# Performance work log

Hardware: AMD Instinct MI355X
Metric: run time of the kernel (lower is better)

Reference implementation:

```python
import jax, jax.numpy as jnp
import numpy as np

N = 50000        # nodes
E = 1600000      # edges (before self loops)
IN_DIM = 300     # input feature size
HID = 256        # hidden size
HEADS = 8
OC = HID // HEADS  # out channels per head = 32
LAYERS = 4
B = 1024         # number of target pairs
C = 3            # num classes
NEG_SLOPE = 0.2  # PyG GATConv leaky_relu slope


def setup_inputs() -> dict:
    key = jax.random.key(0)
    ks = jax.random.split(key, 12)

    def glorot(k, shape):
        lim = np.sqrt(6.0 / (shape[-2] + shape[-1]))
        return jax.random.uniform(k, shape, jnp.float32, -lim, lim)

    return {
        "x": jax.random.normal(ks[0], (N, IN_DIM), jnp.float32),
        "edge_index": jax.random.randint(ks[1], (2, E), 0, N, jnp.int64 if jax.config.jax_enable_x64 else jnp.int32),
        "target_mask": jax.random.randint(ks[2], (B, 2), 0, N, jnp.int64 if jax.config.jax_enable_x64 else jnp.int32),
        # lin1: [IN_DIM, HID] (stored pre-transposed vs torch)
        "lin1_W": glorot(ks[3], (IN_DIM, HID)),
        "lin1_b": jnp.zeros((HID,), jnp.float32),
        # stacked GATConv params
        "convs_W": glorot(ks[4], (LAYERS, HID, HEADS * OC)),
        "convs_att_dst": glorot(ks[5], (LAYERS, HEADS, OC)),  # att half applied to x_i (target)
        "convs_att_src": glorot(ks[6], (LAYERS, HEADS, OC)),  # att half applied to x_j (source)
        "convs_b": jnp.zeros((LAYERS, HID), jnp.float32),
        # lin3: [2*HID, C]
        "lin3_W": glorot(ks[7], (2 * HID, C)),
        "lin3_b": jnp.zeros((C,), jnp.float32),
    }


def gat_layer(h, src, tgt, W, att_dst, att_src, bias):
    """PyG-style GATConv (concat heads), edge list already includes self loops.
    h: [N, HID]; src/tgt: [E+N]; W: [HID, HEADS*OC]."""
    hw = (h @ W).reshape(N, HEADS, OC)
    # per-node attention scores, gathered per-edge (avoids materializing concat features)
    s_dst = jnp.einsum("nho,ho->nh", hw, att_dst)  # score for target role
    s_src = jnp.einsum("nho,ho->nh", hw, att_src)  # score for source role
    alpha = jax.nn.leaky_relu(s_dst[tgt] + s_src[src], NEG_SLOPE)  # [Etot, HEADS]
    # softmax over edges sharing the same target node (self loops => no empty segments)
    m = jax.ops.segment_max(alpha, tgt, num_segments=N)
    ex = jnp.exp(alpha - m[tgt])
    denom = jax.ops.segment_sum(ex, tgt, num_segments=N)
    a = ex / (denom[tgt] + 1e-16)
    # weighted scatter-aggregate of source features
    out = jax.ops.segment_sum(hw[src] * a[:, :, None], tgt, num_segments=N)  # [N, HEADS, OC]
    return out.reshape(N, HEADS * OC) + bias


def reference(x, edge_index, target_mask, lin1_W, lin1_b, convs_W,
              convs_att_dst, convs_att_src, convs_b, lin3_W, lin3_b):
    # add self loops once (PyG GATConv does this per layer; same edge set every layer)
    loop = jnp.arange(N, dtype=edge_index.dtype)
    src = jnp.concatenate([edge_index[0], loop])
    tgt = jnp.concatenate([edge_index[1], loop])

    h = x @ lin1_W + lin1_b
    for l in range(LAYERS):
        h = jax.nn.elu(gat_layer(h, src, tgt, convs_W[l],
                                 convs_att_dst[l], convs_att_src[l], convs_b[l]))
    # gather the two target nodes per sample and flatten -> [B, 2*HID]
    feats = h[target_mask].reshape(B, 2 * HID)
    logits = feats @ lin3_W + lin3_b
    return logits
```

## Files before the change

### kernel.cpp

```cpp
#include <hip/hip_runtime.h>
#include <math.h>

#define N_NODES 50000
#define N_PAD   50048
#define E_EDGES 1600000
#define ETOT    (E_EDGES + N_NODES)
#define EPAD    (E_EDGES + 8 * N_NODES)
#define IN_DIM  300
#define KP1     320
#define HID     256
#define HEADS   8
#define OC      32
#define LAYERS  4
#define BSAMP   1024
#define NEG_SLOPE 0.2f
#define DEG_CAP 128

#define NB     8
#define NPB    6250
#define BCAP   262144
#define NBLK_P 512
#define NBLK_S 196
#define NBLK_B 2048
#define NAGG   2048

typedef unsigned long long ull;
typedef _Float16 half8 __attribute__((ext_vector_type(8)));
typedef _Float16 half4v __attribute__((ext_vector_type(4)));
typedef float f32x4 __attribute__((ext_vector_type(4)));

#define GLDS16(g, l) __builtin_amdgcn_global_load_lds( \
    (const __attribute__((address_space(1))) void*)(g), \
    (__attribute__((address_space(3))) void*)(l), 16, 0, 0)


__global__ __launch_bounds__(256) void part_count_kernel(const int* __restrict__ tgt,
                                                         int* __restrict__ gcount) {
    __shared__ int cnt[NB];
    if (threadIdx.x < NB) cnt[threadIdx.x] = 0;
    __syncthreads();
    const int chunk = (ETOT + NBLK_P - 1) / NBLK_P;
    int beg = blockIdx.x * chunk;
    int end = min(beg + chunk, ETOT);
    for (int e = beg + threadIdx.x; e < end; e += 256) {
        int t_ = (e < E_EDGES) ? tgt[e] : (e - E_EDGES);
        atomicAdd(&cnt[t_ / NPB], 1);
    }
    __syncthreads();
    if (threadIdx.x < NB) gcount[blockIdx.x * NB + threadIdx.x] = cnt[threadIdx.x];
}

__global__ __launch_bounds__(512) void part_scan_kernel(const int* __restrict__ gcount,
                                                        int* __restrict__ goff,
                                                        int* __restrict__ bcnt) {
    __shared__ int arr[NBLK_P][NB];
    int k = threadIdx.x;
    int4 a = ((const int4*)gcount)[k * 2];
    int4 b = ((const int4*)gcount)[k * 2 + 1];
    int own[NB] = {a.x, a.y, a.z, a.w, b.x, b.y, b.z, b.w};
    #pragma unroll
    for (int j = 0; j < NB; j++) arr[k][j] = own[j];
    __syncthreads();
    for (int off = 1; off < NBLK_P; off <<= 1) {
        int tmp[NB];
        #pragma unroll
        for (int j = 0; j < NB; j++) tmp[j] = (k >= off) ? arr[k - off][j] : 0;
        __syncthreads();
        #pragma unroll
        for (int j = 0; j < NB; j++) arr[k][j] += tmp[j];
        __syncthreads();
    }
    int ex[NB];
    #pragma unroll
    for (int j = 0; j < NB; j++) ex[j] = arr[k][j] - own[j];
    ((int4*)goff)[k * 2]     = make_int4(ex[0], ex[1], ex[2], ex[3]);
    ((int4*)goff)[k * 2 + 1] = make_int4(ex[4], ex[5], ex[6], ex[7]);
    if (k == NBLK_P - 1) {
        #pragma unroll
        for (int j = 0; j < NB; j++) bcnt[j] = arr[k][j];
    }
}

__global__ __launch_bounds__(256) void part_scatter_kernel(const int* __restrict__ src,
                                                           const int* __restrict__ tgt,
                                                           const int* __restrict__ goff,
                                                           ull* __restrict__ bpart) {
    __shared__ int cur[NB];
    if (threadIdx.x < NB) cur[threadIdx.x] = goff[blockIdx.x * NB + threadIdx.x];
    __syncthreads();
    const int chunk = (ETOT + NBLK_P - 1) / NBLK_P;
    int beg = blockIdx.x * chunk;
    int end = min(beg + chunk, ETOT);
    for (int e = beg + threadIdx.x; e < end; e += 256) {
        int s_, t_;
        if (e < E_EDGES) { s_ = src[e]; t_ = tgt[e]; }
        else             { s_ = t_ = e - E_EDGES; }
        int b = t_ / NPB;
        int pos = atomicAdd(&cur[b], 1);
        bpart[(size_t)b * BCAP + pos] = ((ull)(unsigned)t_ << 32) | (unsigned)s_;
    }
}

__global__ __launch_bounds__(256) void count_edges_kernel(const ull* __restrict__ bpart,
                                                          const int* __restrict__ bcnt,
                                                          int* counts) {
    int b = blockIdx.x & (NB - 1);
    int ib = blockIdx.x >> 3;
    int nblk = gridDim.x >> 3;
    int nb = bcnt[b];
    const ull* bp = bpart + (size_t)b * BCAP;
    for (int i = ib * 256 + threadIdx.x; i < nb; i += nblk * 256)
        atomicAdd(&counts[(int)(bp[i] >> 32)], 1);
}

__global__ __launch_bounds__(256) void scan1_kernel(const int* __restrict__ counts,
                                                    int* __restrict__ row_ptr,
                                                    int* __restrict__ bsum) {
    __shared__ int sums[256];
    int t = threadIdx.x;
    int i = blockIdx.x * 256 + t;
    int c = (i < N_NODES) ? ((counts[i] + 7) & ~7) : 0;
    sums[t] = c;
    __syncthreads();
    for (int off = 1; off < 256; off <<= 1) {
        int a = sums[t];
        int u = (t >= off) ? sums[t - off] : 0;
        __syncthreads();
        sums[t] = a + u;
        __syncthreads();
    }
    if (i < N_NODES) row_ptr[i] = sums[t] - c;
    if (t == 255) bsum[blockIdx.x] = sums[255];
}

__global__ __launch_bounds__(256) void scan2_kernel(const int* __restrict__ bsum,
                                                    int* __restrict__ boff,
                                                    int* __restrict__ row_ptr) {
    __shared__ int sums[256];
    int t = threadIdx.x;
    int b = (t < NBLK_S) ? bsum[t] : 0;
    sums[t] = b;
    __syncthreads();
    for (int off = 1; off < 256; off <<= 1) {
        int a = sums[t];
        int u = (t >= off) ? sums[t - off] : 0;
        __syncthreads();
        sums[t] = a + u;
        __syncthreads();
    }
    if (t < NBLK_S) boff[t] = sums[t] - b;
    if (t == 255) row_ptr[N_NODES] = sums[255];
}

__global__ __launch_bounds__(256) void scan3_kernel(int* __restrict__ row_ptr,
                                                    const int* __restrict__ boff,
                                                    int* __restrict__ cursor) {
    int i = blockIdx.x * 256 + threadIdx.x;
    if (i >= N_NODES) return;
    int v = row_ptr[i] + boff[blockIdx.x];
    row_ptr[i] = v;
    cursor[i]  = v;
}

__global__ __launch_bounds__(256) void fill_edges_kernel(const ull* __restrict__ bpart,
                                                         const int* __restrict__ bcnt,
                                                         int* cursor, int* __restrict__ col) {
    int b = blockIdx.x & (NB - 1);
    int ib = blockIdx.x >> 3;
    int nblk = gridDim.x >> 3;
    int nb = bcnt[b];
    const ull* bp = bpart + (size_t)b * BCAP;
    for (int i = ib * 256 + threadIdx.x; i < nb; i += nblk * 256) {
        ull pk = bp[i];
        int t_ = (int)(pk >> 32);
        int s_ = (int)pk;
        int pos = atomicAdd(&cursor[t_], 1);
        col[pos] = s_;
    }
}

__global__ __launch_bounds__(256) void pad_edges_kernel(const int* __restrict__ cursor,
                                                        const int* __restrict__ row_ptr,
                                                        int* __restrict__ col) {
    int i = blockIdx.x * 256 + threadIdx.x;
    if (i >= N_NODES) return;
    int e = cursor[i];
    int pe = row_ptr[i + 1];
    for (; e < pe; e++) col[e] = i;
}


__global__ __launch_bounds__(256) void cast_x_kernel(const float* __restrict__ x, _Float16* __restrict__ xh) {
    int i = blockIdx.x * 256 + threadIdx.x;
    if (i >= N_NODES * (KP1 / 8)) return;
    int r = i / (KP1 / 8), c8 = i % (KP1 / 8);
    half8 o;
    const float4* xr = (const float4*)(x + (size_t)r * IN_DIM);
    if (c8 < 37) {
        float4 u = xr[c8 * 2], v = xr[c8 * 2 + 1];
        o[0] = (_Float16)u.x; o[1] = (_Float16)u.y; o[2] = (_Float16)u.z; o[3] = (_Float16)u.w;
        o[4] = (_Float16)v.x; o[5] = (_Float16)v.y; o[6] = (_Float16)v.z; o[7] = (_Float16)v.w;
    } else if (c8 == 37) {
        float4 u = xr[74];
        o[0] = (_Float16)u.x; o[1] = (_Float16)u.y; o[2] = (_Float16)u.z; o[3] = (_Float16)u.w;
        o[4] = o[5] = o[6] = o[7] = (_Float16)0.f;
    } else {
        #pragma unroll
        for (int j = 0; j < 8; j++) o[j] = (_Float16)0.f;
    }
    ((half8*)xh)[i] = o;
}

__global__ __launch_bounds__(256) void cast_w1_kernel(const float* __restrict__ W, _Float16* __restrict__ Wt) {
    int i = blockIdx.x * 256 + threadIdx.x;
    if (i >= HID * KP1) return;
    int n = i / KP1, k = i % KP1;
    float v = (k < IN_DIM) ? W[(size_t)k * HID + n] : 0.f;
    Wt[i] = (_Float16)v;
}

__global__ __launch_bounds__(256) void cast_wc_kernel(const float* __restrict__ W, _Float16* __restrict__ Wt) {
    int i = blockIdx.x * 256 + threadIdx.x;
    if (i >= LAYERS * HID * HID) return;
    int l = i / (HID * HID);
    int r = i % (HID * HID);
    int n = r / HID, k = r % HID;
    Wt[i] = (_Float16)W[(size_t)l * HID * HID + (size_t)k * HID + n];
}

__global__ __launch_bounds__(256) void gemm_mfma_kernel(const _Float16* __restrict__ A,
                                                        const _Float16* __restrict__ Wt,
                                                        const float* __restrict__ bias,
                                                        _Float16* __restrict__ C,
                                                        int M, int Kp, int addbias) {
    __shared__ _Float16 As[128][32];
    __shared__ _Float16 Bs[128][32];
    const int tid = threadIdx.x;
    const int m0 = blockIdx.x * 128;
    const int n0 = blockIdx.y * 128;
    const int w = tid >> 6, lane = tid & 63;
    const int wm = (w & 1) * 64, wn = (w >> 1) * 64;
    const int quad = lane >> 4, m16 = lane & 15;

    f32x4 acc[4][4];
    #pragma unroll
    for (int i = 0; i < 4; i++)
        #pragma unroll
        for (int j = 0; j < 4; j++)
            acc[i][j] = (f32x4){0.f, 0.f, 0.f, 0.f};

    char* lA = (char*)&As[0][0] + w * 1024;
    char* lB = (char*)&Bs[0][0] + w * 1024;

    for (int k0 = 0; k0 < Kp; k0 += 32) {
        #pragma unroll
        for (int i = 0; i < 2; i++) {
            int seg = tid + i * 256;
            int row = seg >> 2, off = seg & 3;
            GLDS16(&A[(size_t)(m0 + row) * Kp + k0 + off * 8], lA + i * 4096);
            GLDS16(&Wt[(size_t)(n0 + row) * Kp + k0 + off * 8], lB + i * 4096);
        }
        __syncthreads();

        half8 af[4], bf[4];
        #pragma unroll
        for (int i = 0; i < 4; i++) {
            af[i] = *(const half8*)&As[wm + i * 16 + m16][quad * 8];
            bf[i] = *(const half8*)&Bs[wn + i * 16 + m16][quad * 8];
        }
        #pragma unroll
        for (int mi = 0; mi < 4; mi++)
            #pragma unroll
            for (int ni = 0; ni < 4; ni++)
                acc[mi][ni] = __builtin_amdgcn_mfma_f32_16x16x32_f16(af[mi], bf[ni], acc[mi][ni], 0, 0, 0);
        __syncthreads();
    }

    #pragma unroll
    for (int mi = 0; mi < 4; mi++) {
        #pragma unroll
        for (int r = 0; r < 4; r++) {
            int row = m0 + wm + mi * 16 + quad * 4 + r;
            if (row < M) {
                #pragma unroll
                for (int ni = 0; ni < 4; ni++) {
                    int colg = n0 + wn + ni * 16 + m16;
                    float v = acc[mi][ni][r];
                    if (addbias) v += bias[colg];
                    C[(size_t)row * HID + colg] = (_Float16)v;
                }
            }
        }
    }
}

__global__ __launch_bounds__(256) void score_kernel(const _Float16* __restrict__ hw,
                                                    const float* __restrict__ att_dst,
                                                    const float* __restrict__ att_src,
                                                    float* __restrict__ s_dst,
                                                    float* __restrict__ s_src) {
    int wv = threadIdx.x >> 6, lane = threadIdx.x & 63;
    int nd = lane >> 3, hd = lane & 7;
    float4 ad[8], as4[8];
    const float4* A4d = (const float4*)att_dst;
    const float4* A4s = (const float4*)att_src;
    #pragma unroll
    for (int j = 0; j < 8; j++) { ad[j] = A4d[hd * 8 + j]; as4[j] = A4s[hd * 8 + j]; }
    const half8* hw8 = (const half8*)hw;
    int nwaves = gridDim.x * 4;
    for (int g = blockIdx.x * 4 + wv; g < N_NODES / 8; g += nwaves) {
        int node = g * 8 + nd;
        float sd = 0.f, ss = 0.f;
        #pragma unroll
        for (int k = 0; k < 4; k++) {
            half8 v = hw8[(size_t)node * 32 + hd * 4 + k];
            #pragma unroll
            for (int i = 0; i < 8; i++) {
                float f = (float)v[i];
                int q = k * 8 + i;
                sd += f * ((const float*)&ad[q >> 2])[q & 3];
                ss += f * ((const float*)&as4[q >> 2])[q & 3];
            }
        }
        s_dst[(size_t)g * 64 + lane] = sd;
        s_src[(size_t)g * 64 + lane] = ss;
    }
}

__global__ __launch_bounds__(256) void agg_kernel(const int* __restrict__ row_ptr,
                                                  const int* __restrict__ deg_arr,
                                                  const int* __restrict__ col,
                                                  const float* __restrict__ s_dst,
                                                  const float* __restrict__ s_src,
                                                  const _Float16* __restrict__ hw,
                                                  const float* __restrict__ bias,
                                                  _Float16* __restrict__ h_out) {
    const int wv   = threadIdx.x >> 6;
    const int lane = threadIdx.x & 63;
    const int bkt  = blockIdx.x & (NB - 1);
    const int ib   = blockIdx.x >> 3;
    const int p  = lane >> 5;
    const int c  = lane & 31;
    const int hh = c >> 2;
    const half8* hw8 = (const half8*)hw;

    f32x4 b0 = ((const f32x4*)bias)[c * 2];
    f32x4 b1 = ((const f32x4*)bias)[c * 2 + 1];

    for (int t0 = ib * 4 + wv; t0 < NPB; t0 += (NAGG / NB) * 4) {
        int t = bkt * NPB + t0;
        int start = row_ptr[t];
        int pdeg  = row_ptr[t + 1] - start;
        int deg   = deg_arr[t];

        if (pdeg <= DEG_CAP) {
            float sdC = s_dst[(size_t)t * HEADS + hh];
            int ngrp = pdeg >> 3;
            const int* cb = col + start;
            float dsum = 0.f;
            float acc[8] = {0.f, 0.f, 0.f, 0.f, 0.f, 0.f, 0.f, 0.f};

            int s0 = cb[p], s1 = cb[2 + p], s2 = cb[4 + p], s3 = cb[6 + p];

            for (int g = 0; g < ngrp; g++) {
                int base = g * 8;
                int n0 = s0, n1 = s1, n2 = s2, n3 = s3;
                if (g + 1 < ngrp) {
                    const int* nb_ = cb + base + 8;
                    n0 = nb_[p]; n1 = nb_[2 + p]; n2 = nb_[4 + p]; n3 = nb_[6 + p];
                }
                float ss0 = s_src[(size_t)s0 * HEADS + hh];
                float ss1 = s_src[(size_t)s1 * HEADS + hh];
                float ss2 = s_src[(size_t)s2 * HEADS + hh];
                float ss3 = s_src[(size_t)s3 * HEADS + hh];
                half8 v0 = hw8[(size_t)s0 * 32 + c];
                half8 v1 = hw8[(size_t)s1 * 32 + c];
                half8 v2 = hw8[(size_t)s2 * 32 + c];
                half8 v3 = hw8[(size_t)s3 * 32 + c];

                float a0 = sdC + ss0; a0 = (a0 > 0.f) ? a0 : NEG_SLOPE * a0;
                float a1 = sdC + ss1; a1 = (a1 > 0.f) ? a1 : NEG_SLOPE * a1;
                float a2 = sdC + ss2; a2 = (a2 > 0.f) ? a2 : NEG_SLOPE * a2;
                float a3 = sdC + ss3; a3 = (a3 > 0.f) ? a3 : NEG_SLOPE * a3;
                float e0 = (base + 0 + p < deg) ? __expf(a0) : 0.f;
                float e1 = (base + 2 + p < deg) ? __expf(a1) : 0.f;
                float e2 = (base + 4 + p < deg) ? __expf(a2) : 0.f;
                float e3 = (base + 6 + p < deg) ? __expf(a3) : 0.f;
                dsum += (e0 + e1) + (e2 + e3);

                #pragma unroll
                for (int i = 0; i < 8; i++)
                    acc[i] += e0 * (float)v0[i] + e1 * (float)v1[i]
                            + e2 * (float)v2[i] + e3 * (float)v3[i];

                s0 = n0; s1 = n1; s2 = n2; s3 = n3;
            }

            dsum += __shfl_xor(dsum, 32);
            float inv = 1.f / (dsum + 1e-16f);
            #pragma unroll
            for (int i = 0; i < 8; i++) acc[i] += __shfl_xor(acc[i], 32);

            if (p == 0) {
                half8 ov;
                #pragma unroll
                for (int i = 0; i < 8; i++) {
                    float bb = (i < 4) ? ((const float*)&b0)[i] : ((const float*)&b1)[i - 4];
                    float o = acc[i] * inv + bb;
                    o = (o > 0.f) ? o : (__expf(o) - 1.f);
                    ov[i] = (_Float16)o;
                }
                ((half8*)h_out)[(size_t)t * 32 + c] = ov;
            }
        } else {
            int eh  = lane & 7;
            int ech = lane >> 3;
            float sd = s_dst[(size_t)t * HEADS + eh];
            int end = start + deg;
            float mx = -1e30f;
            for (int base = start; base < end; base += 8) {
                int e = base + ech;
                if (e < end) {
                    int sn = col[e];
                    float a = sd + s_src[(size_t)sn * HEADS + eh];
                    a = (a > 0.f) ? a : NEG_SLOPE * a;
                    mx = fmaxf(mx, a);
                }
            }
            mx = fmaxf(mx, __shfl_xor(mx, 8));
            mx = fmaxf(mx, __shfl_xor(mx, 16));
            mx = fmaxf(mx, __shfl_xor(mx, 32));

            float4 acc = {0.f, 0.f, 0.f, 0.f};
            float dsum = 0.f;
            const half4v* hw4 = (const half4v*)hw;
            int chead = lane >> 3;
            for (int base = start; base < end; base += 8) {
                int e = base + ech;
                float exv = 0.f;
                int sn = 0;
                if (e < end) {
                    sn = col[e];
                    float a = sd + s_src[(size_t)sn * HEADS + eh];
                    a = (a > 0.f) ? a : NEG_SLOPE * a;
                    exv = __expf(a - mx);
                    dsum += exv;
                }
                int cnt = min(8, end - base);
                for (int j = 0; j < cnt; j++) {
                    float exj = __shfl(exv, j * 8 + chead);
                    int  snj  = __shfl(sn,  j * 8);
                    half4v v = hw4[(size_t)snj * 64 + lane];
                    acc.x += exj * (float)v[0];
                    acc.y += exj * (float)v[1];
                    acc.z += exj * (float)v[2];
                    acc.w += exj * (float)v[3];
                }
            }
            dsum += __shfl_xor(dsum, 8);
            dsum += __shfl_xor(dsum, 16);
            dsum += __shfl_xor(dsum, 32);
            float den = __shfl(dsum, chead) + 1e-16f;
            float inv = 1.f / den;
            int cb = lane * 4;
            float o[4] = {acc.x * inv + bias[cb + 0], acc.y * inv + bias[cb + 1],
                          acc.z * inv + bias[cb + 2], acc.w * inv + bias[cb + 3]};
            #pragma unroll
            for (int i = 0; i < 4; i++) o[i] = (o[i] > 0.f) ? o[i] : (__expf(o[i]) - 1.f);
            half4v ov;
            ov[0] = (_Float16)o[0]; ov[1] = (_Float16)o[1];
            ov[2] = (_Float16)o[2]; ov[3] = (_Float16)o[3];
            ((half4v*)h_out)[(size_t)t * 64 + lane] = ov;
        }
    }
}

__global__ __launch_bounds__(256) void head_kernel(const _Float16* __restrict__ h,
                                                   const int* __restrict__ target_mask,
                                                   const float* __restrict__ W,
                                                   const float* __restrict__ b,
                                                   float* __restrict__ out) {
    int s = blockIdx.x;
    int t = threadIdx.x;
    int n0 = target_mask[s * 2 + 0];
    int n1 = target_mask[s * 2 + 1];
    float f0 = (float)h[(size_t)n0 * HID + t];
    float f1 = (float)h[(size_t)n1 * HID + t];
    float a0 = f0 * W[t * 3 + 0] + f1 * W[(t + 256) * 3 + 0];
    float a1 = f0 * W[t * 3 + 1] + f1 * W[(t + 256) * 3 + 1];
    float a2 = f0 * W[t * 3 + 2] + f1 * W[(t + 256) * 3 + 2];
    #pragma unroll
    for (int off = 32; off >= 1; off >>= 1) {
        a0 += __shfl_xor(a0, off);
        a1 += __shfl_xor(a1, off);
        a2 += __shfl_xor(a2, off);
    }
    __shared__ float red[4][3];
    int wv = t >> 6, ln = t & 63;
    if (ln == 0) { red[wv][0] = a0; red[wv][1] = a1; red[wv][2] = a2; }
    __syncthreads();
    if (t < 3) {
        out[s * 3 + t] = red[0][t] + red[1][t] + red[2][t] + red[3][t] + b[t];
    }
}


extern "C" void kernel_launch(void* const* d_in, const int* in_sizes, int n_in,
                              void* d_out, int out_size, void* d_ws, size_t ws_size,
                              hipStream_t stream) {
    const float* x        = (const float*)d_in[0];
    const int*   eidx     = (const int*)  d_in[1];
    const int*   tmask    = (const int*)  d_in[2];
    const float* lin1_W   = (const float*)d_in[3];
    const float* lin1_b   = (const float*)d_in[4];
    const float* convs_W  = (const float*)d_in[5];
    const float* att_dst  = (const float*)d_in[6];
    const float* att_src  = (const float*)d_in[7];
    const float* convs_b  = (const float*)d_in[8];
    const float* lin3_W   = (const float*)d_in[9];
    const float* lin3_b   = (const float*)d_in[10];
    float* out = (float*)d_out;

    char* ws = (char*)d_ws;
    size_t off = 0;
    auto alloc = [&](size_t bytes) -> void* {
        void* p = ws + off;
        off = (off + bytes + 255) & ~(size_t)255;
        return p;
    };
    _Float16* xh   = (_Float16*)alloc((size_t)N_PAD * KP1 * 2);
    _Float16* h    = (_Float16*)alloc((size_t)N_PAD * HID * 2);
    _Float16* hw   = (_Float16*)alloc((size_t)N_NODES * HID * 2);
    _Float16* w1t  = (_Float16*)alloc((size_t)HID * KP1 * 2);
    _Float16* wct  = (_Float16*)alloc((size_t)LAYERS * HID * HID * 2);
    float* sdst    = (float*)alloc((size_t)N_NODES * HEADS * 4);
    float* ssrc    = (float*)alloc((size_t)N_NODES * HEADS * 4);
    int*   counts  = (int*)  alloc((size_t)N_NODES * 4);
    int*   rowptr  = (int*)  alloc((size_t)(N_NODES + 1) * 4);
    int*   cursor  = (int*)  alloc((size_t)N_NODES * 4);
    int*   col     = (int*)  alloc((size_t)EPAD * 4);
    ull*   bpart   = (ull*)  alloc((size_t)NB * BCAP * 8);
    int*   bcnt    = (int*)  alloc((size_t)NB * 4);
    int*   gcount  = (int*)  alloc((size_t)NBLK_P * NB * 4);
    int*   goff    = (int*)  alloc((size_t)NBLK_P * NB * 4);
    int*   bsum    = (int*)  alloc((size_t)NBLK_S * 4);
    int*   boff    = (int*)  alloc((size_t)NBLK_S * 4);

    const int* src = eidx;
    const int* tgt = eidx + E_EDGES;

    hipMemsetAsync(counts, 0, (size_t)N_NODES * 4, stream);
    part_count_kernel<<<NBLK_P, 256, 0, stream>>>(tgt, gcount);
    part_scan_kernel<<<1, NBLK_P, 0, stream>>>(gcount, goff, bcnt);
    part_scatter_kernel<<<NBLK_P, 256, 0, stream>>>(src, tgt, goff, bpart);
    count_edges_kernel<<<NBLK_B, 256, 0, stream>>>(bpart, bcnt, counts);
    scan1_kernel<<<NBLK_S, 256, 0, stream>>>(counts, rowptr, bsum);
    scan2_kernel<<<1, 256, 0, stream>>>(bsum, boff, rowptr);
    scan3_kernel<<<NBLK_S, 256, 0, stream>>>(rowptr, boff, cursor);
    fill_edges_kernel<<<NBLK_B, 256, 0, stream>>>(bpart, bcnt, cursor, col);
    pad_edges_kernel<<<(N_NODES + 255) / 256, 256, 0, stream>>>(cursor, rowptr, col);

    cast_x_kernel<<<(N_NODES * (KP1 / 8) + 255) / 256, 256, 0, stream>>>(x, xh);
    cast_w1_kernel<<<(HID * KP1 + 255) / 256, 256, 0, stream>>>(lin1_W, w1t);
    cast_wc_kernel<<<(LAYERS * HID * HID + 255) / 256, 256, 0, stream>>>(convs_W, wct);

    gemm_mfma_kernel<<<dim3((N_NODES + 127) / 128, HID / 128), 256, 0, stream>>>(
        xh, w1t, lin1_b, h, N_NODES, KP1, 1);

    for (int l = 0; l < LAYERS; l++) {
        gemm_mfma_kernel<<<dim3((N_NODES + 127) / 128, HID / 128), 256, 0, stream>>>(
            h, wct + (size_t)l * HID * HID, nullptr, hw, N_NODES, HID, 0);
        score_kernel<<<256, 256, 0, stream>>>(
            hw, att_dst + (size_t)l * HEADS * OC, att_src + (size_t)l * HEADS * OC, sdst, ssrc);
        agg_kernel<<<NAGG, 256, 0, stream>>>(
            rowptr, counts, col, sdst, ssrc, hw, convs_b + (size_t)l * HID, h);
    }

    head_kernel<<<BSAMP, 256, 0, stream>>>(h, tmask, lin3_W, lin3_b, out);
}
```

Baseline: 955.6 us.

## Store projected features head-major and aggregate per head with 16-bit column indices

The layer GEMM now writes hw in head-major layout, and the attention scores are stored the same way. The aggregation kernel assigns each block to one head, with 16 edges handled in parallel by 4 lanes each, so each gathered source row is a contiguous 64-byte slice of a smaller per-head working set. Column indices are narrowed to 16-bit, which halves index traffic. The separate high-degree path, which subtracted the max before the softmax, is removed, so every node now takes the unshifted exp path; this risks overflow for large scores, and the column list is re-read once per head.

```diff
diff --git a/kernel.cpp b/kernel.cpp
--- a/kernel.cpp
+++ b/kernel.cpp
@@ -14,7 +14,6 @@
 #define LAYERS  4
 #define BSAMP   1024
 #define NEG_SLOPE 0.2f
-#define DEG_CAP 128
 
 #define NB     8
 #define NPB    6250
@@ -25,8 +24,8 @@
 #define NAGG   2048
 
 typedef unsigned long long ull;
+typedef unsigned short u16;
 typedef _Float16 half8 __attribute__((ext_vector_type(8)));
-typedef _Float16 half4v __attribute__((ext_vector_type(4)));
 typedef float f32x4 __attribute__((ext_vector_type(4)));
 
 #define GLDS16(g, l) __builtin_amdgcn_global_load_lds( \
@@ -164,7 +163,7 @@
 
 __global__ __launch_bounds__(256) void fill_edges_kernel(const ull* __restrict__ bpart,
                                                          const int* __restrict__ bcnt,
-                                                         int* cursor, int* __restrict__ col) {
+                                                         int* cursor, u16* __restrict__ col) {
     int b = blockIdx.x & (NB - 1);
     int ib = blockIdx.x >> 3;
     int nblk = gridDim.x >> 3;
@@ -175,18 +174,18 @@
         int t_ = (int)(pk >> 32);
         int s_ = (int)pk;
         int pos = atomicAdd(&cursor[t_], 1);
-        col[pos] = s_;
+        col[pos] = (u16)s_;
     }
 }
 
 __global__ __launch_bounds__(256) void pad_edges_kernel(const int* __restrict__ cursor,
                                                         const int* __restrict__ row_ptr,
-                                                        int* __restrict__ col) {
+                                                        u16* __restrict__ col) {
     int i = blockIdx.x * 256 + threadIdx.x;
     if (i >= N_NODES) return;
     int e = cursor[i];
     int pe = row_ptr[i + 1];
-    for (; e < pe; e++) col[e] = i;
+    for (; e < pe; e++) col[e] = (u16)i;
 }
 
 
@@ -232,7 +231,8 @@
                                                         const _Float16* __restrict__ Wt,
                                                         const float* __restrict__ bias,
                                                         _Float16* __restrict__ C,
-                                                        int M, int Kp, int addbias) {
+                                                        int M, int Kp, int addbias,
+                                                        int headmajor) {
     __shared__ _Float16 As[128][32];
     __shared__ _Float16 Bs[128][32];
     const int tid = threadIdx.x;
@@ -287,7 +287,12 @@
                     int colg = n0 + wn + ni * 16 + m16;
                     float v = acc[mi][ni][r];
                     if (addbias) v += bias[colg];
-                    C[(size_t)row * HID + colg] = (_Float16)v;
+                    if (headmajor) {
+                        int hd = colg >> 5, oc = colg & 31;
+                        C[((size_t)hd * N_NODES + row) * 32 + oc] = (_Float16)v;
+                    } else {
+                        C[(size_t)row * HID + colg] = (_Float16)v;
+                    }
                 }
             }
         }
@@ -313,7 +318,7 @@
         float sd = 0.f, ss = 0.f;
         #pragma unroll
         for (int k = 0; k < 4; k++) {
-            half8 v = hw8[(size_t)node * 32 + hd * 4 + k];
+            half8 v = hw8[((size_t)hd * N_NODES + node) * 4 + k];
             #pragma unroll
             for (int i = 0; i < 8; i++) {
                 float f = (float)v[i];
@@ -322,14 +327,14 @@
                 ss += f * ((const float*)&as4[q >> 2])[q & 3];
             }
         }
-        s_dst[(size_t)g * 64 + lane] = sd;
-        s_src[(size_t)g * 64 + lane] = ss;
+        s_dst[(size_t)hd * N_NODES + node] = sd;
+        s_src[(size_t)hd * N_NODES + node] = ss;
     }
 }
 
 __global__ __launch_bounds__(256) void agg_kernel(const int* __restrict__ row_ptr,
                                                   const int* __restrict__ deg_arr,
-                                                  const int* __restrict__ col,
+                                                  const u16* __restrict__ col,
                                                   const float* __restrict__ s_dst,
                                                   const float* __restrict__ s_src,
                                                   const _Float16* __restrict__ hw,
@@ -337,140 +342,68 @@
                                                   _Float16* __restrict__ h_out) {
     const int wv   = threadIdx.x >> 6;
     const int lane = threadIdx.x & 63;
-    const int bkt  = blockIdx.x & (NB - 1);
+    const int head = blockIdx.x & (NB - 1);
     const int ib   = blockIdx.x >> 3;
-    const int p  = lane >> 5;
-    const int c  = lane & 31;
-    const int hh = c >> 2;
-    const half8* hw8 = (const half8*)hw;
-
-    f32x4 b0 = ((const f32x4*)bias)[c * 2];
-    f32x4 b1 = ((const f32x4*)bias)[c * 2 + 1];
-
-    for (int t0 = ib * 4 + wv; t0 < NPB; t0 += (NAGG / NB) * 4) {
-        int t = bkt * NPB + t0;
+    const int es = lane >> 2;
+    const int cq = lane & 3;
+    const int wid = ib * 4 + wv;
+    const int NW  = (NAGG / NB) * 4;
+
+    const float* sdh = s_dst + (size_t)head * N_NODES;
+    const float* ssh = s_src + (size_t)head * N_NODES;
+    const half8* hw8 = (const half8*)(hw + (size_t)head * N_NODES * 32);
+
+    f32x4 b0 = ((const f32x4*)bias)[head * 8 + cq * 2];
+    f32x4 b1 = ((const f32x4*)bias)[head * 8 + cq * 2 + 1];
+
+    for (int t = wid; t < N_NODES; t += NW) {
         int start = row_ptr[t];
         int pdeg  = row_ptr[t + 1] - start;
         int deg   = deg_arr[t];
-
-        if (pdeg <= DEG_CAP) {
-            float sdC = s_dst[(size_t)t * HEADS + hh];
-            int ngrp = pdeg >> 3;
-            const int* cb = col + start;
-            float dsum = 0.f;
-            float acc[8] = {0.f, 0.f, 0.f, 0.f, 0.f, 0.f, 0.f, 0.f};
-
-            int s0 = cb[p], s1 = cb[2 + p], s2 = cb[4 + p], s3 = cb[6 + p];
-
-            for (int g = 0; g < ngrp; g++) {
-                int base = g * 8;
-                int n0 = s0, n1 = s1, n2 = s2, n3 = s3;
-                if (g + 1 < ngrp) {
-                    const int* nb_ = cb + base + 8;
-                    n0 = nb_[p]; n1 = nb_[2 + p]; n2 = nb_[4 + p]; n3 = nb_[6 + p];
-                }
-                float ss0 = s_src[(size_t)s0 * HEADS + hh];
-                float ss1 = s_src[(size_t)s1 * HEADS + hh];
-                float ss2 = s_src[(size_t)s2 * HEADS + hh];
-                float ss3 = s_src[(size_t)s3 * HEADS + hh];
-                half8 v0 = hw8[(size_t)s0 * 32 + c];
-                half8 v1 = hw8[(size_t)s1 * 32 + c];
-                half8 v2 = hw8[(size_t)s2 * 32 + c];
-                half8 v3 = hw8[(size_t)s3 * 32 + c];
-
-                float a0 = sdC + ss0; a0 = (a0 > 0.f) ? a0 : NEG_SLOPE * a0;
-                float a1 = sdC + ss1; a1 = (a1 > 0.f) ? a1 : NEG_SLOPE * a1;
-                float a2 = sdC + ss2; a2 = (a2 > 0.f) ? a2 : NEG_SLOPE * a2;
-                float a3 = sdC + ss3; a3 = (a3 > 0.f) ? a3 : NEG_SLOPE * a3;
-                float e0 = (base + 0 + p < deg) ? __expf(a0) : 0.f;
-                float e1 = (base + 2 + p < deg) ? __expf(a1) : 0.f;
-                float e2 = (base + 4 + p < deg) ? __expf(a2) : 0.f;
-                float e3 = (base + 6 + p < deg) ? __expf(a3) : 0.f;
-                dsum += (e0 + e1) + (e2 + e3);
-
-                #pragma unroll
-                for (int i = 0; i < 8; i++)
-                    acc[i] += e0 * (float)v0[i] + e1 * (float)v1[i]
-                            + e2 * (float)v2[i] + e3 * (float)v3[i];
-
-                s0 = n0; s1 = n1; s2 = n2; s3 = n3;
+        const u16* cb = col + start;
+        float sdv = sdh[t];
+
+        int ngrp = (pdeg + 15) >> 4;
+        float dsum = 0.f;
+        float acc[8] = {0.f, 0.f, 0.f, 0.f, 0.f, 0.f, 0.f, 0.f};
+
+        int sn = (es < pdeg) ? (int)cb[es] : 0;
+        for (int g = 0; g < ngrp; g++) {
+            int base = g * 16;
+            int nsl = base + 16 + es;
+            int snN = (nsl < pdeg) ? (int)cb[nsl] : 0;
+
+            float ss = ssh[sn];
+            half8 v = hw8[(size_t)sn * 4 + cq];
+
+            float a = sdv + ss;
+            a = (a > 0.f) ? a : NEG_SLOPE * a;
+            float e = (base + es < deg) ? __expf(a) : 0.f;
+            dsum += e;
+            #pragma unroll
+            for (int i = 0; i < 8; i++) acc[i] += e * (float)v[i];
+
+            sn = snN;
+        }
+
+        #pragma unroll
+        for (int off = 4; off <= 32; off <<= 1) {
+            dsum += __shfl_xor(dsum, off);
+            #pragma unroll
+            for (int i = 0; i < 8; i++) acc[i] += __shfl_xor(acc[i], off);
+        }
+
+        if (es == 0) {
+            float inv = 1.f / (dsum + 1e-16f);
+            half8 ov;
+            #pragma unroll
+            for (int i = 0; i < 8; i++) {
+                float bb = (i < 4) ? ((const float*)&b0)[i] : ((const float*)&b1)[i - 4];
+                float o = acc[i] * inv + bb;
+                o = (o > 0.f) ? o : (__expf(o) - 1.f);
+                ov[i] = (_Float16)o;
             }
-
-            dsum += __shfl_xor(dsum, 32);
-            float inv = 1.f / (dsum + 1e-16f);
-            #pragma unroll
-            for (int i = 0; i < 8; i++) acc[i] += __shfl_xor(acc[i], 32);
-
-            if (p == 0) {
-                half8 ov;
-                #pragma unroll
-                for (int i = 0; i < 8; i++) {
-                    float bb = (i < 4) ? ((const float*)&b0)[i] : ((const float*)&b1)[i - 4];
-                    float o = acc[i] * inv + bb;
-                    o = (o > 0.f) ? o : (__expf(o) - 1.f);
-                    ov[i] = (_Float16)o;
-                }
-                ((half8*)h_out)[(size_t)t * 32 + c] = ov;
-            }
-        } else {
-            int eh  = lane & 7;
-            int ech = lane >> 3;
-            float sd = s_dst[(size_t)t * HEADS + eh];
-            int end = start + deg;
-            float mx = -1e30f;
-            for (int base = start; base < end; base += 8) {
-                int e = base + ech;
-                if (e < end) {
-                    int sn = col[e];
-                    float a = sd + s_src[(size_t)sn * HEADS + eh];
-                    a = (a > 0.f) ? a : NEG_SLOPE * a;
-                    mx = fmaxf(mx, a);
-                }
-            }
-            mx = fmaxf(mx, __shfl_xor(mx, 8));
-            mx = fmaxf(mx, __shfl_xor(mx, 16));
-            mx = fmaxf(mx, __shfl_xor(mx, 32));
-
-            float4 acc = {0.f, 0.f, 0.f, 0.f};
-            float dsum = 0.f;
-            const half4v* hw4 = (const half4v*)hw;
-            int chead = lane >> 3;
-            for (int base = start; base < end; base += 8) {
-                int e = base + ech;
-                float exv = 0.f;
-                int sn = 0;
-                if (e < end) {
-                    sn = col[e];
-                    float a = sd + s_src[(size_t)sn * HEADS + eh];
-                    a = (a > 0.f) ? a : NEG_SLOPE * a;
-                    exv = __expf(a - mx);
-                    dsum += exv;
-                }
-                int cnt = min(8, end - base);
-                for (int j = 0; j < cnt; j++) {
-                    float exj = __shfl(exv, j * 8 + chead);
-                    int  snj  = __shfl(sn,  j * 8);
-                    half4v v = hw4[(size_t)snj * 64 + lane];
-                    acc.x += exj * (float)v[0];
-                    acc.y += exj * (float)v[1];
-                    acc.z += exj * (float)v[2];
-                    acc.w += exj * (float)v[3];
-                }
-            }
-            dsum += __shfl_xor(dsum, 8);
-            dsum += __shfl_xor(dsum, 16);
-            dsum += __shfl_xor(dsum, 32);
-            float den = __shfl(dsum, chead) + 1e-16f;
-            float inv = 1.f / den;
-            int cb = lane * 4;
-            float o[4] = {acc.x * inv + bias[cb + 0], acc.y * inv + bias[cb + 1],
-                          acc.z * inv + bias[cb + 2], acc.w * inv + bias[cb + 3]};
-            #pragma unroll
-            for (int i = 0; i < 4; i++) o[i] = (o[i] > 0.f) ? o[i] : (__expf(o[i]) - 1.f);
-            half4v ov;
-            ov[0] = (_Float16)o[0]; ov[1] = (_Float16)o[1];
-            ov[2] = (_Float16)o[2]; ov[3] = (_Float16)o[3];
-            ((half4v*)h_out)[(size_t)t * 64 + lane] = ov;
+            ((half8*)h_out)[(size_t)t * 32 + head * 4 + cq] = ov;
         }
     }
 }
@@ -530,15 +463,15 @@
     };
     _Float16* xh   = (_Float16*)alloc((size_t)N_PAD * KP1 * 2);
     _Float16* h    = (_Float16*)alloc((size_t)N_PAD * HID * 2);
-    _Float16* hw   = (_Float16*)alloc((size_t)N_NODES * HID * 2);
+    _Float16* hw   = (_Float16*)alloc((size_t)N_PAD * HID * 2);
     _Float16* w1t  = (_Float16*)alloc((size_t)HID * KP1 * 2);
     _Float16* wct  = (_Float16*)alloc((size_t)LAYERS * HID * HID * 2);
-    float* sdst    = (float*)alloc((size_t)N_NODES * HEADS * 4);
-    float* ssrc    = (float*)alloc((size_t)N_NODES * HEADS * 4);
+    float* sdst    = (float*)alloc((size_t)HEADS * N_NODES * 4);
+    float* ssrc    = (float*)alloc((size_t)HEADS * N_NODES * 4);
     int*   counts  = (int*)  alloc((size_t)N_NODES * 4);
     int*   rowptr  = (int*)  alloc((size_t)(N_NODES + 1) * 4);
     int*   cursor  = (int*)  alloc((size_t)N_NODES * 4);
-    int*   col     = (int*)  alloc((size_t)EPAD * 4);
+    u16*   col     = (u16*)  alloc((size_t)(EPAD + 32) * 2);
     ull*   bpart   = (ull*)  alloc((size_t)NB * BCAP * 8);
     int*   bcnt    = (int*)  alloc((size_t)NB * 4);
     int*   gcount  = (int*)  alloc((size_t)NBLK_P * NB * 4);
@@ -565,11 +498,11 @@
     cast_wc_kernel<<<(LAYERS * HID * HID + 255) / 256, 256, 0, stream>>>(convs_W, wct);
 
     gemm_mfma_kernel<<<dim3((N_NODES + 127) / 128, HID / 128), 256, 0, stream>>>(
-        xh, w1t, lin1_b, h, N_NODES, KP1, 1);
+        xh, w1t, lin1_b, h, N_NODES, KP1, 1, 0);
 
     for (int l = 0; l < LAYERS; l++) {
         gemm_mfma_kernel<<<dim3((N_NODES + 127) / 128, HID / 128), 256, 0, stream>>>(
-            h, wct + (size_t)l * HID * HID, nullptr, hw, N_NODES, HID, 0);
+            h, wct + (size_t)l * HID * HID, nullptr, hw, N_NODES, HID, 0, 1);
         score_kernel<<<256, 256, 0, stream>>>(
             hw, att_dst + (size_t)l * HEADS * OC, att_src + (size_t)l * HEADS * OC, sdst, ssrc);
         agg_kernel<<<NAGG, 256, 0, stream>>>(
```

New measurement: 1.243 ms. +30.0%, slower.
